# Kernel tuning notes

Measured on AMD Instinct MI355X. Metric: run time of the kernel, lower is better.

## Reference

```python
import jax, jax.numpy as jnp
import numpy as np

B, L, D, NH, NITEMS = 256, 200, 128, 2, 100000
HD = D // NH
LAMB = 0.6
NEG = -1e9

_PARAM_SHAPES = dict(
    item_emb=(NITEMS, D), pos_emb=(L, D),
    W_ei=(D, D), b_ei=(D,), W_eo=(D, D), b_eo=(D,), b_iah=(D,), b_oah=(D,),
    w_ih=(3 * D, 2 * D), b_ih=(3 * D,), w_hh=(3 * D, D), b_hh=(3 * D,),
    ln1_g=(D,), ln1_b=(D,),
    Wq=(D, D), bq=(D,), Wk=(D, D), bk=(D,), Wv=(D, D), bv=(D,), Wo=(D, D), bo=(D,),
    ln2_g=(D,), ln2_b=(D,), W1=(D, D), b1=(D,), W2=(D, D), b2=(D,),
    lnf_g=(D,), lnf_b=(D,),
)


def setup_inputs() -> dict:
    key = jax.random.key(0)
    ks = jax.random.split(key, len(_PARAM_SHAPES) + 2)
    stdv = 1.0 / np.sqrt(D)  # GCSAN._init_weights: uniform(-stdv, stdv) on ALL params
    p = {}
    for i, (name, shp) in enumerate(_PARAM_SHAPES.items()):
        p[name] = jax.random.uniform(ks[i], shp, jnp.float32, -stdv, stdv)
    lens = jax.random.randint(ks[-2], (B,), L // 4, L + 1)
    vals = jax.random.randint(ks[-1], (B, L), 1, NITEMS)
    # trailing zero padding, as the original break-on-zero loop assumes
    seqs = jnp.where(jnp.arange(L)[None, :] < lens[:, None], vals, 0).astype(jnp.int32)
    p['seqs'] = seqs
    p['lens'] = lens.astype(jnp.int32)
    return p


def _ln(x, g, b):
    mu = x.mean(-1, keepdims=True)
    var = ((x - mu) ** 2).mean(-1, keepdims=True)
    return (x - mu) / jnp.sqrt(var + 1e-5) * g + b


def _build_graph(seqs):
    # Vectorized replacement of _get_slice (per-row np.unique + adjacency build)
    def per_row(seq):
        s = jnp.sort(seq)
        first = jnp.concatenate([jnp.ones((1,), bool), s[1:] != s[:-1]])
        pos = jnp.cumsum(first) - 1  # compaction target of each first-occurrence
        items = jnp.zeros((L,), seq.dtype).at[jnp.where(first, pos, L)].set(s, mode='drop')
        n_u = first.sum()
        search = jnp.where(jnp.arange(L) < n_u, items, jnp.iinfo(jnp.int32).max)
        alias = jnp.searchsorted(search, seq).astype(jnp.int32)
        return items, alias
    items, alias = jax.vmap(per_row)(seqs)
    valid = seqs[:, 1:] > 0  # edge (i -> i+1) exists until first pad
    u = jnp.where(valid, alias[:, :-1], L)  # route masked edges to dummy row L
    v = jnp.where(valid, alias[:, 1:], L)
    bidx = jnp.arange(B)[:, None]
    uA = jnp.zeros((B, L + 1, L + 1), jnp.float32).at[bidx, u, v].set(1.0)[:, :L, :L]
    in_deg = jnp.maximum(uA.sum(1), 1.0)
    out_deg = jnp.maximum(uA.sum(2), 1.0)
    A_in = jnp.swapaxes(uA, 1, 2) / in_deg[:, :, None]   # A[i,j] = uA[j,i]/in_deg[i]
    A_out = uA / out_deg[:, :, None]                     # A[i,k] = uA[i,k]/out_deg[i]
    return alias, jnp.concatenate([A_in, A_out], axis=2), items  # A: [B, L, 2L]


def reference(item_emb, pos_emb, W_ei, b_ei, W_eo, b_eo, b_iah, b_oah,
              w_ih, b_ih, w_hh, b_hh, ln1_g, ln1_b, Wq, bq, Wk, bk, Wv, bv,
              Wo, bo, ln2_g, ln2_b, W1, b1, W2, b2, lnf_g, lnf_b, seqs, lens):
    alias, A, items = _build_graph(seqs)
    hidden = item_emb[items]  # [B, L, D]
    # SR-GNN gated cell, step = n_layers = 1
    for _ in range(1):
        h_in = jnp.einsum('bij,bjd->bid', A[:, :, :L], hidden @ W_ei.T + b_ei) + b_iah
        h_out = jnp.einsum('bij,bjd->bid', A[:, :, L:], hidden @ W_eo.T + b_eo) + b_oah
        gi = jnp.concatenate([h_in, h_out], -1) @ w_ih.T + b_ih
        gh = hidden @ w_hh.T + b_hh
        i_r, i_i, i_n = jnp.split(gi, 3, -1)
        h_r, h_i, h_n = jnp.split(gh, 3, -1)
        r = jax.nn.sigmoid(i_r + h_r)
        z = jax.nn.sigmoid(i_i + h_i)
        ng = jnp.tanh(i_n + r * h_n)
        hidden = ng + z * (hidden - ng)
    bidx = jnp.arange(B)
    seq_hidden = hidden[bidx[:, None], alias]  # alias-gather back to sequence order
    last_idx = lens - 1
    ht = seq_hidden[bidx, last_idx]
    x = seq_hidden + pos_emb[None, :, :]
    tl_mask = (seqs > 0)[:, :, None].astype(x.dtype)
    x = x * tl_mask
    causal = jnp.triu(jnp.ones((L, L), bool), 1)  # True = masked future (bidirectional=False)
    # SASRec-style block: ln -> MHA residual -> ln -> pointwise FFN residual
    q_in = _ln(x, ln1_g, ln1_b)
    heads = lambda t: t.reshape(B, L, NH, HD).transpose(0, 2, 1, 3)
    q = heads(q_in @ Wq.T + bq)
    k = heads(x @ Wk.T + bk)
    v = heads(x @ Wv.T + bv)
    sc = jnp.einsum('bhqd,bhkd->bhqk', q, k) / jnp.sqrt(jnp.asarray(HD, x.dtype))
    sc = jnp.where(causal[None, None], NEG, sc)
    attn = jax.nn.softmax(sc, -1)
    mo = jnp.einsum('bhqk,bhkd->bhqd', attn, v).transpose(0, 2, 1, 3).reshape(B, L, D) @ Wo.T + bo
    x = q_in + mo
    h = _ln(x, ln2_g, ln2_b)
    x = h + jax.nn.relu(h @ W1.T + b1) @ W2.T + b2
    x = x * tl_mask
    log_feats = _ln(x, lnf_g, lnf_b)
    out = log_feats[bidx, last_idx]
    return LAMB * out + (1.0 - LAMB) * ht
```

## Files before the change

kernel.cpp:

```cpp
#include <hip/hip_runtime.h>
#include <hip/hip_bf16.h>

#define Bb 256
#define Ll 200
#define Dd 128
#define BL (Bb*Ll)

typedef __hip_bfloat16 bf16;
typedef __attribute__((ext_vector_type(8))) short short8;
typedef __attribute__((ext_vector_type(4))) unsigned short ushort4v;
typedef __attribute__((ext_vector_type(4))) float floatx4;

__device__ __forceinline__ float b2f(bf16 v) { return __bfloat162float(v); }
__device__ __forceinline__ bf16  f2b(float v) { return __float2bfloat16(v); }
__device__ __forceinline__ float us2f(unsigned short u) { return __uint_as_float(((unsigned)u) << 16); }
__device__ __forceinline__ unsigned short f2us(float v) { bf16 t = f2b(v); return *(unsigned short*)&t; }
__device__ __forceinline__ float ldf(const void* p, int i, int f32) {
  return f32 ? ((const float*)p)[i] : b2f(((const bf16*)p)[i]);
}
__device__ __forceinline__ int detect_f32(const unsigned short* __restrict__ w) {
  unsigned short u = w[threadIdx.x & 63];
  return (__ballot(((u >> 7) & 0xFF) >= 0x7F) != 0ull) ? 1 : 0;
}
__device__ __forceinline__ void load_lds16(const void* g, void* l) {
  __builtin_amdgcn_global_load_lds((const __attribute__((address_space(1))) unsigned int*)g,
                                   (__attribute__((address_space(3))) unsigned int*)l, 16, 0, 0);
}

struct PackP {
  const void *W_ei,*W_eo,*w_ih,*w_hh,*Wk,*Wv,*Wqp,*Wop,*W1p,*W2p,*pos;
  const void *b_ei,*b_eo,*b_ih,*b_hh,*bk,*bv,*bqp,*bop,*b1p,*b2p,*biah,*boah;
  const void *ln1g,*ln1b,*ln2g,*ln2b,*lnfg,*lnfb;
  bf16 *cWhe,*cWih,*cWhh,*cWkv,*cWq,*cWo,*cW1,*cW2,*cPos;
  float *bias_he,*bias_gi,*bias_gh,*bias_kv,*cbq,*cbo,*cb1,*cb2,*cbiah,*cboah,*cln;
  const int* seqs;
  int *alias_g, *items_g; float *rin_g, *rout_g; unsigned *adj_g, *adjT_g;
};
__global__ __launch_bounds__(256) void k01(PackP p) {
  __shared__ int s[Ll], al[Ll], its[Ll];
  __shared__ unsigned char isf[Ll];
  __shared__ unsigned adjL[Ll*8], adjTL[Ll*8];
  if (blockIdx.x < 1199) {
    int idx = blockIdx.x * 256 + threadIdx.x;
    int f32 = detect_f32((const unsigned short*)p.W_ei);
    if (idx < 131072) {
      if (idx < 32768) {
        int r = idx >> 7, c = idx & 127;
        p.cWhe[idx] = f2b(r < 128 ? ldf(p.W_ei, r*128+c, f32) : ldf(p.W_eo, (r-128)*128+c, f32));
      } else p.cWih[idx-32768] = f2b(ldf(p.w_ih, idx-32768, f32));
    } else if (idx < 278528) {
      if (idx < 180224)      p.cWhh[idx-131072] = f2b(ldf(p.w_hh, idx-131072, f32));
      else if (idx < 212992) {
        int i = idx - 180224; int r = i >> 7, c = i & 127;
        p.cWkv[i] = f2b(r < 128 ? ldf(p.Wk, r*128+c, f32) : ldf(p.Wv, (r-128)*128+c, f32));
      }
      else if (idx < 229376) p.cWq[idx-212992] = f2b(ldf(p.Wqp, idx-212992, f32));
      else if (idx < 245760) p.cWo[idx-229376] = f2b(ldf(p.Wop, idx-229376, f32));
      else if (idx < 262144) p.cW1[idx-245760] = f2b(ldf(p.W1p, idx-245760, f32));
      else                   p.cW2[idx-262144] = f2b(ldf(p.W2p, idx-262144, f32));
    } else if (idx < 304128) {
      p.cPos[idx-278528] = f2b(ldf(p.pos, idx-278528, f32));
    } else {
      int j = idx - 304128;
      if      (j < 256)  p.bias_he[j]     = (j<128) ? ldf(p.b_ei,j,f32) : ldf(p.b_eo,j-128,f32);
      else if (j < 640)  p.bias_gi[j-256] = ldf(p.b_ih, j-256, f32);
      else if (j < 1024) p.bias_gh[j-640] = ldf(p.b_hh, j-640, f32);
      else if (j < 1280) { int c=j-1024; p.bias_kv[c] = (c<128)? ldf(p.bk,c,f32): ldf(p.bv,c-128,f32); }
      else if (j < 1408) p.cbq[j-1280]   = ldf(p.bqp, j-1280, f32);
      else if (j < 1536) p.cbo[j-1408]   = ldf(p.bop, j-1408, f32);
      else if (j < 1664) p.cb1[j-1536]   = ldf(p.b1p, j-1536, f32);
      else if (j < 1792) p.cb2[j-1664]   = ldf(p.b2p, j-1664, f32);
      else if (j < 1920) p.cbiah[j-1792] = ldf(p.biah, j-1792, f32);
      else if (j < 2048) p.cboah[j-1920] = ldf(p.boah, j-1920, f32);
      else {
        int i = j - 2048, g = i >> 7, c2 = i & 127;
        const void* s6 = g==0?p.ln1g: g==1?p.ln1b: g==2?p.ln2g: g==3?p.ln2b: g==4?p.lnfg: p.lnfb;
        p.cln[i] = ldf(s6, c2, f32);
      }
    }
    return;
  }
  int b = blockIdx.x - 1199, t = threadIdx.x;
  if (t < Ll) s[t] = p.seqs[b*Ll + t];
  for (int i = t; i < Ll*8; i += 256) { adjL[i] = 0u; adjTL[i] = 0u; }
  __syncthreads();
  if (t < Ll) {
    int v = s[t]; bool f = true;
    for (int j = 0; j < t; j++) if (s[j] == v) { f = false; break; }
    isf[t] = f ? 1 : 0; its[t] = 0;
  }
  __syncthreads();
  if (t < Ll) {
    int v = s[t], r = 0;
    for (int j = 0; j < Ll; j++) r += (isf[j] && s[j] < v);
    al[t] = r;
  }
  __syncthreads();
  if (t < Ll && isf[t]) its[al[t]] = s[t];
  if (t < Ll-1 && s[t+1] > 0) {
    int u = al[t], v = al[t+1];
    atomicOr(&adjL [u*8 + (v >> 5)], 1u << (v & 31));
    atomicOr(&adjTL[v*8 + (u >> 5)], 1u << (u & 31));
  }
  __syncthreads();
  if (t < Ll) {
    int od = 0, id = 0;
    for (int wd = 0; wd < 7; wd++) { od += __popc(adjL[t*8+wd]); id += __popc(adjTL[t*8+wd]); }
    p.rout_g [b*Ll + t] = 1.0f / (float)max(od, 1);
    p.rin_g  [b*Ll + t] = 1.0f / (float)max(id, 1);
    p.alias_g[b*Ll + t] = al[t];
    p.items_g[b*Ll + t] = its[t];
  }
  for (int i = t; i < Ll*8; i += 256) { p.adj_g[b*Ll*8 + i] = adjL[i]; p.adjT_g[b*Ll*8 + i] = adjTL[i]; }
}

__global__ __launch_bounds__(256) void k2_gather(const void* __restrict__ emb, const void* __restrict__ wei,
    const int* __restrict__ items_g, bf16* __restrict__ hidden)
{
  int idx = blockIdx.x * 256 + threadIdx.x;
  int f32 = detect_f32((const unsigned short*)wei);
  int n = idx >> 4, jv = idx & 15;
  int it = items_g[n];
  short8 o;
  if (f32) {
    const float* e = (const float*)emb + (size_t)it * 128 + jv * 8;
#pragma unroll
    for (int j = 0; j < 8; j++) o[j] = (short)f2us(e[j]);
  } else {
    o = ((const short8*)((const bf16*)emb + (size_t)it * 128))[jv];
  }
  ((short8*)hidden)[idx] = o;
}

template<int K>
__global__ __launch_bounds__(256) void gemm6(const bf16* __restrict__ A, const bf16* __restrict__ W,
    const float* __restrict__ bias,
    bf16* __restrict__ out_lo, int Nlo, bf16* __restrict__ out_hi, int Nhi, int split)
{
  __shared__ short As[128*128];
  __shared__ short Ws[128*128];
  int t = threadIdx.x;
  int wave = t >> 6, lane = t & 63;
  int q = lane >> 4, mr = lane & 15;
  int wm = wave & 1, wn = wave >> 1;
  int m0 = blockIdx.x * 128, n0 = blockIdx.y * 128;
  int srow = lane >> 4;
  int c16 = lane & 15;
  floatx4 acc[4][4] = {};
  for (int k0 = 0; k0 < K; k0 += 128) {
#pragma unroll
    for (int i = 0; i < 8; i++) {
      int seg = wave*8 + i;
      int r = seg*4 + srow;
      int gch = c16 ^ (r & 15);
      load_lds16(A + (size_t)(m0 + r) * K + k0 + gch*8, &As[seg*512]);
      load_lds16(W + (size_t)(n0 + r) * K + k0 + gch*8, &Ws[seg*512]);
    }
    __syncthreads();
#pragma unroll
    for (int kk = 0; kk < 4; kk++) {
      short8 af[4], wf[4];
#pragma unroll
      for (int i = 0; i < 4; i++) {
        int row = wm*64 + i*16 + mr;
        af[i] = *(const short8*)(&As[row*128 + ((kk*4+q) ^ (row&15))*8]);
      }
#pragma unroll
      for (int j = 0; j < 4; j++) {
        int row = wn*64 + j*16 + mr;
        wf[j] = *(const short8*)(&Ws[row*128 + ((kk*4+q) ^ (row&15))*8]);
      }
#pragma unroll
      for (int i = 0; i < 4; i++)
#pragma unroll
        for (int j = 0; j < 4; j++)
          acc[i][j] = __builtin_amdgcn_mfma_f32_16x16x32_bf16(wf[j], af[i], acc[i][j], 0, 0, 0);
    }
    if (k0 + 128 < K) __syncthreads();
  }
#pragma unroll
  for (int j = 0; j < 4; j++) {
    int ng = n0 + wn*64 + j*16 + q*4;
    floatx4 bs = *(const floatx4*)(bias + ng);
    bf16* outp; int col, stride;
    if (ng < split) { outp = out_lo; col = ng; stride = Nlo; }
    else            { outp = out_hi; col = ng - split; stride = Nhi; }
#pragma unroll
    for (int i = 0; i < 4; i++) {
      int m = m0 + wm*64 + i*16 + mr;
      ushort4v o;
#pragma unroll
      for (int e = 0; e < 4; e++) o[e] = f2us(acc[i][j][e] + bs[e]);
      *(ushort4v*)(outp + (size_t)m * stride + col) = o;
    }
  }
}

__global__ __launch_bounds__(256) void k3_agg(const bf16* __restrict__ he,
    const unsigned* __restrict__ adj_g, const unsigned* __restrict__ adjT_g,
    const float* __restrict__ rin_g, const float* __restrict__ rout_g,
    const float* __restrict__ cbiah, const float* __restrict__ cboah, bf16* __restrict__ hio)
{
  int b = blockIdx.x / 25, chunk = blockIdx.x % 25;
  int wave = threadIdx.x >> 6, lane = threadIdx.x & 63;
  bool isIn = lane < 32;
  int c = isIn ? 4*lane : 128 + 4*(lane-32);
  const bf16* heb = he + (size_t)b * Ll * 256;
  bf16* hiob = hio + (size_t)b * Ll * 256;
  float bias0 = isIn ? cbiah[c]   : cboah[c-128];
  float bias1 = isIn ? cbiah[c+1] : cboah[c-127];
  float bias2 = isIn ? cbiah[c+2] : cboah[c-126];
  float bias3 = isIn ? cbiah[c+3] : cboah[c-125];
#pragma unroll
  for (int s = 0; s < 2; s++) {
    int i = chunk*8 + wave + 4*s;
    const unsigned* mrow = (isIn ? adjT_g : adj_g) + ((size_t)b*Ll + i) * 8;
    float a0=0.f, a1=0.f, a2=0.f, a3=0.f;
    for (int wd = 0; wd < 7; wd++) {
      unsigned bits = mrow[wd];
      while (bits) {
        int j = (wd << 5) + __builtin_ctz(bits); bits &= bits - 1;
        ushort4v h4 = *(const ushort4v*)(heb + (size_t)j*256 + c);
        a0 += us2f(h4.x); a1 += us2f(h4.y); a2 += us2f(h4.z); a3 += us2f(h4.w);
      }
    }
    float r = isIn ? rin_g[b*Ll + i] : rout_g[b*Ll + i];
    ushort4v o;
    o.x = f2us(bias0 + r*a0); o.y = f2us(bias1 + r*a1);
    o.z = f2us(bias2 + r*a2); o.w = f2us(bias3 + r*a3);
    *(ushort4v*)(hiob + (size_t)i*256 + c) = o;
  }
}

__global__ __launch_bounds__(256) void k4_gru(const bf16* __restrict__ gi, const bf16* __restrict__ gh,
                                              bf16* __restrict__ hidden)
{
  int idx = blockIdx.x * 256 + threadIdx.x;
  int n = idx >> 4, jv = idx & 15;
  const short8* gin = (const short8*)(gi + (size_t)n * 384);
  const short8* ghn = (const short8*)(gh + (size_t)n * 384);
  short8 vir = gin[jv], vii = gin[16+jv], vnn = gin[32+jv];
  short8 whr = ghn[jv], whi = ghn[16+jv], whn = ghn[32+jv];
  short8 hv  = ((const short8*)hidden)[idx];
  short8 o;
#pragma unroll
  for (int e = 0; e < 8; e++) {
    float ir = us2f((unsigned short)vir[e]), ii = us2f((unsigned short)vii[e]), inn = us2f((unsigned short)vnn[e]);
    float hr = us2f((unsigned short)whr[e]), hi = us2f((unsigned short)whi[e]), hn = us2f((unsigned short)whn[e]);
    float r  = 1.f / (1.f + __expf(-(ir + hr)));
    float z  = 1.f / (1.f + __expf(-(ii + hi)));
    float arg = inn + r * hn;
    float ex = __expf(-2.f * arg);
    float ng = (1.f - ex) / (1.f + ex);
    float h  = us2f((unsigned short)hv[e]);
    o[e] = (short)f2us(ng + z * (h - ng));
  }
  ((short8*)hidden)[idx] = o;
}

__global__ __launch_bounds__(256) void k5_x(const bf16* __restrict__ hidden, const int* __restrict__ alias_g,
    const int* __restrict__ seqs, const int* __restrict__ lens,
    const bf16* __restrict__ cPos, bf16* __restrict__ x, float* __restrict__ ht)
{
  int idx = blockIdx.x * 256 + threadIdx.x;
  int jv = idx & 15; int bt = idx >> 4; int tpos = bt % Ll; int b = bt / Ll;
  int a = alias_g[bt];
  short8 hv = ((const short8*)(hidden + ((size_t)b*Ll + a) * Dd))[jv];
  short8 pv = ((const short8*)(cPos + tpos * Dd))[jv];
  bool valid = seqs[bt] > 0;
  bool isLast = (tpos == lens[b] - 1);
  short8 o;
#pragma unroll
  for (int e = 0; e < 8; e++) {
    float sh = us2f((unsigned short)hv[e]);
    float val = valid ? sh + us2f((unsigned short)pv[e]) : 0.f;
    o[e] = (short)f2us(val);
    if (isLast) ht[b*Dd + jv*8 + e] = sh;
  }
  ((short8*)x)[idx] = o;
}

struct FinalP {
  const bf16 *x, *kv; const float* ht;
  const bf16 *cWq, *cWo, *cW1, *cW2;
  const float *cbq, *cbo, *cb1, *cb2, *cln;
  const int* lens; const void* wei;
  void* out;
};
__device__ __forceinline__ float dot128i(const bf16* __restrict__ wrow, const float* __restrict__ vin) {
  const short8* wr = (const short8*)wrow;
  float a0=0.f, a1=0.f, a2=0.f, a3=0.f;
#pragma unroll
  for (int kk = 0; kk < 4; kk++) {
    short8 w0 = wr[kk*4+0], w1 = wr[kk*4+1], w2 = wr[kk*4+2], w3 = wr[kk*4+3];
#pragma unroll
    for (int j = 0; j < 8; j++) {
      a0 += vin[kk*32 +      j] * us2f((unsigned short)w0[j]);
      a1 += vin[kk*32 + 8  + j] * us2f((unsigned short)w1[j]);
      a2 += vin[kk*32 + 16 + j] * us2f((unsigned short)w2[j]);
      a3 += vin[kk*32 + 24 + j] * us2f((unsigned short)w3[j]);
    }
  }
  return (a0+a1)+(a2+a3);
}
__device__ __forceinline__ float wave_sum(float v) {
#pragma unroll
  for (int m = 1; m < 64; m <<= 1) v += __shfl_xor(v, m, 64);
  return v;
}
__device__ __forceinline__ float wave_max(float v) {
#pragma unroll
  for (int m = 1; m < 64; m <<= 1) v = fmaxf(v, __shfl_xor(v, m, 64));
  return v;
}
__global__ __launch_bounds__(256) void k7_final(FinalP p)
{
  __shared__ float sred[8];
  __shared__ float qin[128], qv[128], aout[128], hh[128], f1[128];
  __shared__ float pb0[256], pb1[256];
  __shared__ floatx4 av4[8][32];
  int b = blockIdx.x, t = threadIdx.x, c = t;
  int w = t >> 6, ln = t & 63;
  int li = p.lens[b] - 1;
  int f32 = detect_f32((const unsigned short*)p.wei);
  float xv = (c < 128) ? b2f(p.x[((size_t)b*Ll + li) * Dd + c]) : 0.f;
  float s = wave_sum(xv), s2 = wave_sum(xv*xv);
  if (ln == 0) { sred[w] = s; sred[4+w] = s2; }
  __syncthreads();
  float mu = (sred[0]+sred[1]+sred[2]+sred[3]) * (1.f/128.f);
  float ms = (sred[4]+sred[5]+sred[6]+sred[7]) * (1.f/128.f);
  float rs = rsqrtf(fmaxf(ms - mu*mu, 0.f) + 1e-5f);
  __syncthreads();
  if (c < 128) qin[c] = (xv - mu) * rs * p.cln[c] + p.cln[128+c];
  __syncthreads();
  if (c < 128) qv[c] = p.cbq[c] + dot128i(p.cWq + c*128, qin);
  __syncthreads();
  const bf16* kvb = p.kv + (size_t)b * Ll * 256;
  float s0 = -3.0e38f, s1 = -3.0e38f;
  if (t <= li) {
    const short8* kr = (const short8*)(kvb + (size_t)t*256);
    float a00=0.f,a01=0.f,a10=0.f,a11=0.f;
#pragma unroll
    for (int kk = 0; kk < 4; kk++) {
      short8 k0 = kr[kk*2], k1 = kr[kk*2+1], k2 = kr[8+kk*2], k3 = kr[8+kk*2+1];
#pragma unroll
      for (int j = 0; j < 8; j++) {
        a00 += qv[kk*16 + j]      * us2f((unsigned short)k0[j]);
        a01 += qv[kk*16 + 8 + j]  * us2f((unsigned short)k1[j]);
        a10 += qv[64 + kk*16 + j]     * us2f((unsigned short)k2[j]);
        a11 += qv[64 + kk*16 + 8 + j] * us2f((unsigned short)k3[j]);
      }
    }
    s0 = (a00+a01) * 0.125f; s1 = (a10+a11) * 0.125f;
  }
  float m0 = wave_max(s0), m1 = wave_max(s1);
  if (ln == 0) { sred[w] = m0; sred[4+w] = m1; }
  __syncthreads();
  m0 = fmaxf(fmaxf(sred[0],sred[1]), fmaxf(sred[2],sred[3]));
  m1 = fmaxf(fmaxf(sred[4],sred[5]), fmaxf(sred[6],sred[7]));
  __syncthreads();
  float e0 = (t <= li) ? __expf(s0 - m0) : 0.f;
  float e1 = (t <= li) ? __expf(s1 - m1) : 0.f;
  pb0[t] = e0; pb1[t] = e1;
  float l0 = wave_sum(e0), l1 = wave_sum(e1);
  if (ln == 0) { sred[w] = l0; sred[4+w] = l1; }
  __syncthreads();
  l0 = sred[0]+sred[1]+sred[2]+sred[3];
  l1 = sred[4]+sred[5]+sred[6]+sred[7];
  {
    int part = t >> 5, cq = t & 31, ch = cq * 4;
    int cnt = li + 1, cpp = (cnt + 7) >> 3;
    int j0 = part * cpp, j1 = min(j0 + cpp, cnt);
    const float* pbh = (ch < 64) ? pb0 : pb1;
    float a0=0.f,a1=0.f,a2=0.f,a3=0.f;
#pragma unroll 4
    for (int j = j0; j < j1; j++) {
      ushort4v v4 = *(const ushort4v*)(kvb + (size_t)j*256 + 128 + ch);
      float pw = pbh[j];
      a0 += pw*us2f(v4.x); a1 += pw*us2f(v4.y); a2 += pw*us2f(v4.z); a3 += pw*us2f(v4.w);
    }
    floatx4 o = {a0,a1,a2,a3};
    av4[part][cq] = o;
  }
  __syncthreads();
  if (c < 128) {
    float l = (c < 64) ? l0 : l1;
    float acc = 0.f;
#pragma unroll
    for (int pp = 0; pp < 8; pp++) acc += ((const float*)&av4[pp][c>>2])[c&3];
    aout[c] = acc / l;
  }
  __syncthreads();
  float x2v = 0.f;
  if (c < 128) x2v = qin[c] + p.cbo[c] + dot128i(p.cWo + c*128, aout);
  s = wave_sum((c<128)?x2v:0.f); s2 = wave_sum((c<128)?x2v*x2v:0.f);
  if (ln == 0) { sred[w] = s; sred[4+w] = s2; }
  __syncthreads();
  mu = (sred[0]+sred[1]+sred[2]+sred[3]) * (1.f/128.f);
  ms = (sred[4]+sred[5]+sred[6]+sred[7]) * (1.f/128.f);
  rs = rsqrtf(fmaxf(ms - mu*mu, 0.f) + 1e-5f);
  __syncthreads();
  if (c < 128) hh[c] = (x2v - mu) * rs * p.cln[256+c] + p.cln[384+c];
  __syncthreads();
  if (c < 128) f1[c] = fmaxf(p.cb1[c] + dot128i(p.cW1 + c*128, hh), 0.f);
  __syncthreads();
  float x3v = 0.f;
  if (c < 128) x3v = hh[c] + p.cb2[c] + dot128i(p.cW2 + c*128, f1);
  s = wave_sum((c<128)?x3v:0.f); s2 = wave_sum((c<128)?x3v*x3v:0.f);
  if (ln == 0) { sred[w] = s; sred[4+w] = s2; }
  __syncthreads();
  mu = (sred[0]+sred[1]+sred[2]+sred[3]) * (1.f/128.f);
  ms = (sred[4]+sred[5]+sred[6]+sred[7]) * (1.f/128.f);
  rs = rsqrtf(fmaxf(ms - mu*mu, 0.f) + 1e-5f);
  if (c < 128) {
    float lf = (x3v - mu) * rs * p.cln[512+c] + p.cln[640+c];
    float outv = 0.6f * lf + 0.4f * p.ht[b*Dd + c];
    if (f32) ((float*)p.out)[b*Dd + c] = outv;
    else     ((bf16*)p.out)[b*Dd + c]  = f2b(outv);
  }
}

extern "C" void kernel_launch(void* const* d_in, const int* in_sizes, int n_in,
                              void* d_out, int out_size, void* d_ws, size_t ws_size,
                              hipStream_t stream)
{
  (void)in_sizes; (void)n_in; (void)out_size; (void)ws_size;
  const void* item_emb = d_in[0];
  const int* seqs = (const int*)d_in[30];
  const int* lens = (const int*)d_in[31];

  char* wsp = (char*)d_ws;
  size_t o = 0;
  auto alloc = [&](size_t sz) { void* p = wsp + o; o += (sz + 255) & ~(size_t)255; return p; };
  int*      alias_g = (int*)alloc((size_t)BL*4);
  int*      items_g = (int*)alloc((size_t)BL*4);
  float*    rin_g   = (float*)alloc((size_t)BL*4);
  float*    rout_g  = (float*)alloc((size_t)BL*4);
  unsigned* adj_g   = (unsigned*)alloc((size_t)BL*8*4);
  unsigned* adjT_g  = (unsigned*)alloc((size_t)BL*8*4);
  float*    ht_g    = (float*)alloc((size_t)Bb*Dd*4);
  bf16*     cWhe    = (bf16*)alloc(32768*2);
  bf16*     cWhh    = (bf16*)alloc(49152*2);
  bf16*     cWih    = (bf16*)alloc(98304*2);
  bf16*     cWkv    = (bf16*)alloc(32768*2);
  bf16*     cWq     = (bf16*)alloc(16384*2);
  bf16*     cWo     = (bf16*)alloc(16384*2);
  bf16*     cW1     = (bf16*)alloc(16384*2);
  bf16*     cW2     = (bf16*)alloc(16384*2);
  bf16*     cPos    = (bf16*)alloc(25600*2);
  float*    bias_he = (float*)alloc(256*4);
  float*    bias_gh = (float*)alloc(384*4);
  float*    bias_gi = (float*)alloc(384*4);
  float*    bias_kv = (float*)alloc(256*4);
  float*    cbq     = (float*)alloc(128*4);
  float*    cbo     = (float*)alloc(128*4);
  float*    cb1     = (float*)alloc(128*4);
  float*    cb2     = (float*)alloc(128*4);
  float*    cbiah   = (float*)alloc(128*4);
  float*    cboah   = (float*)alloc(128*4);
  float*    cln     = (float*)alloc(768*4);
  bf16*     hidden  = (bf16*)alloc((size_t)BL*128*2);
  bf16*     he      = (bf16*)alloc((size_t)BL*256*2);
  bf16*     hio     = (bf16*)alloc((size_t)BL*256*2);
  bf16*     gi      = (bf16*)alloc((size_t)BL*384*2);
  bf16*     gh      = (bf16*)alloc((size_t)BL*384*2);
  bf16*     x  = he;
  bf16*     kv = hio;

  PackP pp = { d_in[2], d_in[4], d_in[8], d_in[10], d_in[16], d_in[18], d_in[14], d_in[20],
               d_in[24], d_in[26], d_in[1],
               d_in[3], d_in[5], d_in[9], d_in[11], d_in[17], d_in[19], d_in[15], d_in[21],
               d_in[25], d_in[27], d_in[6], d_in[7],
               d_in[12], d_in[13], d_in[22], d_in[23], d_in[28], d_in[29],
               cWhe, cWih, cWhh, cWkv, cWq, cWo, cW1, cW2, cPos,
               bias_he, bias_gi, bias_gh, bias_kv, cbq, cbo, cb1, cb2, cbiah, cboah, cln,
               seqs, alias_g, items_g, rin_g, rout_g, adj_g, adjT_g };
  k01<<<1199 + Bb, 256, 0, stream>>>(pp);
  k2_gather<<<BL*16/256, 256, 0, stream>>>(item_emb, d_in[2], items_g, hidden);
  gemm6<128><<<dim3(BL/128, 5), 256, 0, stream>>>(hidden, cWhe, bias_he, he, 256, gh, 384, 256);
  k3_agg<<<Bb*25, 256, 0, stream>>>(he, adj_g, adjT_g, rin_g, rout_g, cbiah, cboah, hio);
  gemm6<256><<<dim3(BL/128, 3), 256, 0, stream>>>(hio, cWih, bias_gi, gi, 384, gi, 384, 1<<30);
  k4_gru<<<BL*16/256, 256, 0, stream>>>(gi, gh, hidden);
  k5_x<<<BL*16/256, 256, 0, stream>>>(hidden, alias_g, seqs, lens, cPos, x, ht_g);
  gemm6<128><<<dim3(BL/128, 2), 256, 0, stream>>>(x, cWkv, bias_kv, kv, 256, kv, 256, 1<<30);
  FinalP fp = { x, kv, ht_g, cWq, cWo, cW1, cW2, cbq, cbo, cb1, cb2, cln, lens, d_in[2], d_out };
  k7_final<<<Bb, 256, 0, stream>>>(fp);
}
```

Measured before the change: 290.6 us.

## Fuse GRU update with alias gather and vectorize graph-build dedup loops

Merges the GRU cell kernel and the alias-gather/positional-add kernel into one kernel per batch half. The updated hidden state stays in shared memory and is gathered from there, so it is never written to and re-read from global memory. The graph-build blocks now take the low block indices, and their duplicate and rank scans read int4/packed words instead of single elements. Each fused kernel launch has only 512 blocks, so occupancy is lower than with the previous element-wise grids.

```diff
diff --git a/kernel.cpp b/kernel.cpp
--- a/kernel.cpp
+++ b/kernel.cpp
@@ -37,11 +37,12 @@
   int *alias_g, *items_g; float *rin_g, *rout_g; unsigned *adj_g, *adjT_g;
 };
 __global__ __launch_bounds__(256) void k01(PackP p) {
-  __shared__ int s[Ll], al[Ll], its[Ll];
-  __shared__ unsigned char isf[Ll];
+  __shared__ alignas(16) int s[Ll];
+  __shared__ int al[Ll], its[Ll];
+  __shared__ alignas(4) unsigned char isf[Ll];
   __shared__ unsigned adjL[Ll*8], adjTL[Ll*8];
-  if (blockIdx.x < 1199) {
-    int idx = blockIdx.x * 256 + threadIdx.x;
+  if (blockIdx.x >= Bb) {
+    int idx = (blockIdx.x - Bb) * 256 + threadIdx.x;
     int f32 = detect_f32((const unsigned short*)p.W_ei);
     if (idx < 131072) {
       if (idx < 32768) {
@@ -80,19 +81,33 @@
     }
     return;
   }
-  int b = blockIdx.x - 1199, t = threadIdx.x;
+  int b = blockIdx.x, t = threadIdx.x;
   if (t < Ll) s[t] = p.seqs[b*Ll + t];
   for (int i = t; i < Ll*8; i += 256) { adjL[i] = 0u; adjTL[i] = 0u; }
   __syncthreads();
+  const int4* s4 = (const int4*)s;
   if (t < Ll) {
-    int v = s[t]; bool f = true;
-    for (int j = 0; j < t; j++) if (s[j] == v) { f = false; break; }
-    isf[t] = f ? 1 : 0; its[t] = 0;
-  }
-  __syncthreads();
+    int v = s[t]; int dup = 0;
+    int nb = t >> 2;
+    for (int j4 = 0; j4 < nb; j4++) {
+      int4 sv = s4[j4];
+      dup |= (sv.x==v) | (sv.y==v) | (sv.z==v) | (sv.w==v);
+    }
+    for (int j = nb*4; j < t; j++) dup |= (s[j]==v);
+    isf[t] = dup ? 0 : 1; its[t] = 0;
+  }
+  __syncthreads();
+  const unsigned* isfw = (const unsigned*)isf;
   if (t < Ll) {
     int v = s[t], r = 0;
-    for (int j = 0; j < Ll; j++) r += (isf[j] && s[j] < v);
+    for (int j4 = 0; j4 < Ll/4; j4++) {
+      int4 sv = s4[j4];
+      unsigned fw = isfw[j4];
+      r += ((fw & 0xffu)       && sv.x < v);
+      r += ((fw & 0xff00u)     && sv.y < v);
+      r += ((fw & 0xff0000u)   && sv.z < v);
+      r += ((fw & 0xff000000u) && sv.w < v);
+    }
     al[t] = r;
   }
   __syncthreads();
@@ -232,52 +247,58 @@
   }
 }
 
-__global__ __launch_bounds__(256) void k4_gru(const bf16* __restrict__ gi, const bf16* __restrict__ gh,
-                                              bf16* __restrict__ hidden)
-{
-  int idx = blockIdx.x * 256 + threadIdx.x;
-  int n = idx >> 4, jv = idx & 15;
-  const short8* gin = (const short8*)(gi + (size_t)n * 384);
-  const short8* ghn = (const short8*)(gh + (size_t)n * 384);
-  short8 vir = gin[jv], vii = gin[16+jv], vnn = gin[32+jv];
-  short8 whr = ghn[jv], whi = ghn[16+jv], whn = ghn[32+jv];
-  short8 hv  = ((const short8*)hidden)[idx];
-  short8 o;
-#pragma unroll
-  for (int e = 0; e < 8; e++) {
-    float ir = us2f((unsigned short)vir[e]), ii = us2f((unsigned short)vii[e]), inn = us2f((unsigned short)vnn[e]);
-    float hr = us2f((unsigned short)whr[e]), hi = us2f((unsigned short)whi[e]), hn = us2f((unsigned short)whn[e]);
-    float r  = 1.f / (1.f + __expf(-(ir + hr)));
-    float z  = 1.f / (1.f + __expf(-(ii + hi)));
-    float arg = inn + r * hn;
-    float ex = __expf(-2.f * arg);
-    float ng = (1.f - ex) / (1.f + ex);
-    float h  = us2f((unsigned short)hv[e]);
-    o[e] = (short)f2us(ng + z * (h - ng));
-  }
-  ((short8*)hidden)[idx] = o;
-}
-
-__global__ __launch_bounds__(256) void k5_x(const bf16* __restrict__ hidden, const int* __restrict__ alias_g,
+__global__ __launch_bounds__(256) void k45(const bf16* __restrict__ gi, const bf16* __restrict__ gh,
+    const bf16* __restrict__ hidden, const int* __restrict__ alias_g,
     const int* __restrict__ seqs, const int* __restrict__ lens,
     const bf16* __restrict__ cPos, bf16* __restrict__ x, float* __restrict__ ht)
 {
-  int idx = blockIdx.x * 256 + threadIdx.x;
-  int jv = idx & 15; int bt = idx >> 4; int tpos = bt % Ll; int b = bt / Ll;
-  int a = alias_g[bt];
-  short8 hv = ((const short8*)(hidden + ((size_t)b*Ll + a) * Dd))[jv];
-  short8 pv = ((const short8*)(cPos + tpos * Dd))[jv];
-  bool valid = seqs[bt] > 0;
-  bool isLast = (tpos == lens[b] - 1);
-  short8 o;
-#pragma unroll
-  for (int e = 0; e < 8; e++) {
-    float sh = us2f((unsigned short)hv[e]);
-    float val = valid ? sh + us2f((unsigned short)pv[e]) : 0.f;
-    o[e] = (short)f2us(val);
-    if (isLast) ht[b*Dd + jv*8 + e] = sh;
-  }
-  ((short8*)x)[idx] = o;
+  __shared__ bf16 hnew[Ll*64];
+  __shared__ int aliasL[Ll];
+  __shared__ unsigned char validL[Ll];
+  int b = blockIdx.x >> 1, half = blockIdx.x & 1;
+  int t = threadIdx.x;
+  if (t < Ll) { aliasL[t] = alias_g[b*Ll + t]; validL[t] = seqs[b*Ll + t] > 0; }
+  int li = lens[b] - 1;
+  for (int u = t; u < Ll*8; u += 256) {
+    int n = u >> 3, grp = u & 7;
+    int j8 = half*8 + grp;
+    const short8* gin = (const short8*)(gi + ((size_t)b*Ll + n) * 384);
+    const short8* ghn = (const short8*)(gh + ((size_t)b*Ll + n) * 384);
+    short8 vir = gin[j8], vii = gin[16+j8], vnn = gin[32+j8];
+    short8 whr = ghn[j8], whi = ghn[16+j8], whn = ghn[32+j8];
+    short8 hv  = ((const short8*)(hidden + ((size_t)b*Ll + n) * Dd))[j8];
+    short8 o;
+#pragma unroll
+    for (int e = 0; e < 8; e++) {
+      float ir = us2f((unsigned short)vir[e]), ii = us2f((unsigned short)vii[e]), inn = us2f((unsigned short)vnn[e]);
+      float hr = us2f((unsigned short)whr[e]), hi = us2f((unsigned short)whi[e]), hn = us2f((unsigned short)whn[e]);
+      float r  = 1.f / (1.f + __expf(-(ir + hr)));
+      float z  = 1.f / (1.f + __expf(-(ii + hi)));
+      float arg = inn + r * hn;
+      float ex = __expf(-2.f * arg);
+      float ng = (1.f - ex) / (1.f + ex);
+      float h  = us2f((unsigned short)hv[e]);
+      o[e] = (short)f2us(ng + z * (h - ng));
+    }
+    *(short8*)&hnew[n*64 + grp*8] = o;
+  }
+  __syncthreads();
+  for (int u = t; u < Ll*8; u += 256) {
+    int tpos = u >> 3, grp = u & 7;
+    int a = aliasL[tpos];
+    short8 sh8 = *(const short8*)&hnew[a*64 + grp*8];
+    short8 pv = ((const short8*)(cPos + tpos * Dd))[half*8 + grp];
+    bool valid = validL[tpos];
+    bool isLast = (tpos == li);
+    short8 o;
+#pragma unroll
+    for (int e = 0; e < 8; e++) {
+      float sh = us2f((unsigned short)sh8[e]);
+      o[e] = valid ? (short)f2us(sh + us2f((unsigned short)pv[e])) : (short)0;
+      if (isLast) ht[b*Dd + half*64 + grp*8 + e] = sh;
+    }
+    ((short8*)(x + ((size_t)b*Ll + tpos) * Dd))[half*8 + grp] = o;
+  }
 }
 
 struct FinalP {
@@ -475,13 +496,12 @@
                cWhe, cWih, cWhh, cWkv, cWq, cWo, cW1, cW2, cPos,
                bias_he, bias_gi, bias_gh, bias_kv, cbq, cbo, cb1, cb2, cbiah, cboah, cln,
                seqs, alias_g, items_g, rin_g, rout_g, adj_g, adjT_g };
-  k01<<<1199 + Bb, 256, 0, stream>>>(pp);
+  k01<<<Bb + 1199, 256, 0, stream>>>(pp);
   k2_gather<<<BL*16/256, 256, 0, stream>>>(item_emb, d_in[2], items_g, hidden);
   gemm6<128><<<dim3(BL/128, 5), 256, 0, stream>>>(hidden, cWhe, bias_he, he, 256, gh, 384, 256);
   k3_agg<<<Bb*25, 256, 0, stream>>>(he, adj_g, adjT_g, rin_g, rout_g, cbiah, cboah, hio);
   gemm6<256><<<dim3(BL/128, 3), 256, 0, stream>>>(hio, cWih, bias_gi, gi, 384, gi, 384, 1<<30);
-  k4_gru<<<BL*16/256, 256, 0, stream>>>(gi, gh, hidden);
-  k5_x<<<BL*16/256, 256, 0, stream>>>(hidden, alias_g, seqs, lens, cPos, x, ht_g);
+  k45<<<Bb*2, 256, 0, stream>>>(gi, gh, hidden, alias_g, seqs, lens, cPos, x, ht_g);
   gemm6<128><<<dim3(BL/128, 2), 256, 0, stream>>>(x, cWkv, bias_kv, kv, 256, kv, 256, 1<<30);
   FinalP fp = { x, kv, ht_g, cWq, cWo, cW1, cW2, cbq, cbo, cb1, cb2, cln, lens, d_in[2], d_out };
   k7_final<<<Bb, 256, 0, stream>>>(fp);
```

Result: faster. 280.1 us (-3.6%).
